# Optimization experiments

Hardware: AMD Instinct MI355X
Metric: run time of the kernel (lower is better)

## Reference

```python
import jax, jax.numpy as jnp
import numpy as np
from jax import lax

RADIUS = 0.25
MAX_NUM_NEIGHBORS = 32
N = 8192
D = 3
NUM_BATCHES = 16


def setup_inputs() -> dict:
    key = jax.random.key(0)
    k1, k2 = jax.random.split(key)
    x = jax.random.uniform(k1, (N, D), dtype=jnp.float32)  # points in unit cube
    batch = jnp.sort(jax.random.randint(k2, (N,), 0, NUM_BATCHES, dtype=jnp.int32))
    return {"x": x, "batch": batch}


def reference(x, batch):
    # radius_graph(x, r, max_num_neighbors=K, batch=batch):
    # for each target point i, up to K source points j (j != i, same batch,
    # ||x_i - x_j|| <= r). Deterministic tie-break: keep the K nearest.
    # Output padded to fixed shape [2, N*K] with -1 for missing edges.
    K = MAX_NUM_NEIGHBORS
    n = x.shape[0]
    sq = jnp.sum(x * x, axis=-1)                      # [N]
    d2 = sq[:, None] + sq[None, :] - 2.0 * (x @ x.T)  # [N, N] squared dists
    same_batch = batch[:, None] == batch[None, :]
    not_self = ~jnp.eye(n, dtype=bool)
    valid = same_batch & not_self & (d2 <= RADIUS * RADIUS)
    masked = jnp.where(valid, d2, jnp.inf)
    neg_vals, idx = lax.top_k(-masked, K)             # K nearest per row
    sel_valid = jnp.isfinite(neg_vals)                # [N, K]
    src = jnp.where(sel_valid, idx, -1)               # neighbor (source) index
    tgt = jnp.where(sel_valid,
                    jnp.broadcast_to(jnp.arange(n, dtype=idx.dtype)[:, None], (n, K)),
                    -1)
    # flow = source_to_target: row 0 = sources (neighbors), row 1 = targets
    edge_index = jnp.stack([src.reshape(-1), tgt.reshape(-1)], axis=0)  # [2, N*K]
    return edge_index
```

## Files before the change

### kernel.cpp

```cpp
#include <hip/hip_runtime.h>
#include <stdint.h>

#define NB   16
#define K    32
#define R2   0.0625f
#define WPB  4
#define MAXC 256

__global__ void radius_prep_kernel(const float* __restrict__ x,
                                   const int* __restrict__ batch,
                                   int n,
                                   int* __restrict__ starts,
                                   float* __restrict__ sq) {
#pragma clang fp contract(off)
    int i = blockIdx.x * blockDim.x + threadIdx.x;
    if (i >= n) return;
    float x0 = x[i * 3 + 0];
    float x1 = x[i * 3 + 1];
    float x2 = x[i * 3 + 2];
    float p0 = x0 * x0;
    float p1 = x1 * x1;
    float p2 = x2 * x2;
    sq[i] = (p0 + p1) + p2;

    int b  = batch[i];
    int bp = (i == 0) ? -1 : batch[i - 1];
    for (int bb = bp + 1; bb <= b; ++bb) starts[bb] = i;
    if (i == n - 1) {
        for (int bb = b + 1; bb <= NB; ++bb) starts[bb] = n;
    }
}

__global__ __launch_bounds__(256) void radius_knn_wave(
    const float* __restrict__ x,
    const int* __restrict__ batch,
    const int* __restrict__ starts,
    const float* __restrict__ sq,
    int n,
    int* __restrict__ out,
    int row_stride ) {
#pragma clang fp contract(off)
    __shared__ uint64_t buf[WPB][MAXC];
    __shared__ int      res[WPB][K];

    const int tid  = threadIdx.x;
    const int lane = tid & 63;
    const int wid  = tid >> 6;
    const int i    = blockIdx.x * WPB + wid;

    const int b = batch[i];
    const int s = starts[b];
    const int e = starts[b + 1];

    const float xi0 = x[i * 3 + 0];
    const float xi1 = x[i * 3 + 1];
    const float xi2 = x[i * 3 + 2];
    const float sqi = sq[i];

    const int range = e - s;
    const int iters = (range + 63) >> 6;
    int cbase = 0;
    for (int it = 0; it < iters; ++it) {
        const int j  = s + it * 64 + lane;
        const int jc = (j < e) ? j : s;
        float y0 = x[jc * 3 + 0];
        float y1 = x[jc * 3 + 1];
        float y2 = x[jc * 3 + 2];
        float dot = xi0 * y0;
        dot = fmaf(xi1, y1, dot);
        dot = fmaf(xi2, y2, dot);
        float d2 = (sqi + sq[jc]) - 2.0f * dot;
        bool pass = (j < e) && (j != i) && (d2 <= R2);

        d2 = d2 + 0.0f;
        uint32_t u = __float_as_uint(d2);
        u = (u & 0x80000000u) ? ~u : (u | 0x80000000u);
        uint64_t key = ((uint64_t)u << 32) | (uint32_t)jc;

        uint64_t mask = __ballot(pass);
        if (pass) {
            int off = cbase + __popcll(mask & ((1ull << lane) - 1ull));
            if (off < MAXC) buf[wid][off] = key;
        }
        cbase += (int)__popcll(mask);
    }
    int cnt = cbase < MAXC ? cbase : MAXC;
    const int nsel = cnt < K ? cnt : K;

    __syncthreads();

    for (int p = lane; p < cnt; p += 64) {
        uint64_t kp = buf[wid][p];
        int r = 0;
        for (int q = 0; q < cnt; ++q)
            r += (buf[wid][q] < kp) ? 1 : 0;
        if (r < K) res[wid][r] = (int)(uint32_t)(kp & 0xffffffffu);
    }

    __syncthreads();

    const long base = (long)i * K;
    if (lane < K) {
        out[base + lane] = (lane < nsel) ? res[wid][lane] : -1;
    } else {
        const int l2 = lane - K;
        out[row_stride + base + l2] = (l2 < nsel) ? i : -1;
    }
}

extern "C" void kernel_launch(void* const* d_in, const int* in_sizes, int n_in,
                              void* d_out, int out_size, void* d_ws, size_t ws_size,
                              hipStream_t stream) {
    const float* x     = (const float*)d_in[0];
    const int*   batch = (const int*)d_in[1];
    const int    n     = in_sizes[1];
    int*         out   = (int*)d_out;
    const int row_stride = out_size / 2;

    int*   starts = (int*)d_ws;
    float* sq     = (float*)((char*)d_ws + 128);

    radius_prep_kernel<<<(n + 255) / 256, 256, 0, stream>>>(x, batch, n, starts, sq);

    const int blocks = n / WPB;
    radius_knn_wave<<<blocks, 256, 0, stream>>>(x, batch, starts, sq, n,
                                                out, row_stride);
}
```

Measured before the change: 17.66 us.

## Fuse prep kernel into main kernel via binary search and inline squared norms

Removes the separate prep kernel launch that computed per-point squared norms and batch start offsets. Each wave now binary-searches the sorted batch array to find its batch range, and squared norms are recomputed on the fly from the coordinates. This saves a kernel launch and the dependency between the two kernels. In exchange it adds redundant per-wave search work and extra ALU work in the inner loop.

```diff
diff --git a/kernel.cpp b/kernel.cpp
--- a/kernel.cpp
+++ b/kernel.cpp
@@ -7,35 +7,9 @@
 #define WPB  4
 #define MAXC 256
 
-__global__ void radius_prep_kernel(const float* __restrict__ x,
-                                   const int* __restrict__ batch,
-                                   int n,
-                                   int* __restrict__ starts,
-                                   float* __restrict__ sq) {
-#pragma clang fp contract(off)
-    int i = blockIdx.x * blockDim.x + threadIdx.x;
-    if (i >= n) return;
-    float x0 = x[i * 3 + 0];
-    float x1 = x[i * 3 + 1];
-    float x2 = x[i * 3 + 2];
-    float p0 = x0 * x0;
-    float p1 = x1 * x1;
-    float p2 = x2 * x2;
-    sq[i] = (p0 + p1) + p2;
-
-    int b  = batch[i];
-    int bp = (i == 0) ? -1 : batch[i - 1];
-    for (int bb = bp + 1; bb <= b; ++bb) starts[bb] = i;
-    if (i == n - 1) {
-        for (int bb = b + 1; bb <= NB; ++bb) starts[bb] = n;
-    }
-}
-
-__global__ __launch_bounds__(256) void radius_knn_wave(
+__global__ __launch_bounds__(256) void radius_knn_fused(
     const float* __restrict__ x,
     const int* __restrict__ batch,
-    const int* __restrict__ starts,
-    const float* __restrict__ sq,
     int n,
     int* __restrict__ out,
     int row_stride ) {
@@ -49,13 +23,25 @@
     const int i    = blockIdx.x * WPB + wid;
 
     const int b = batch[i];
-    const int s = starts[b];
-    const int e = starts[b + 1];
+
+    int lo = 0, hi = n;
+    while (lo < hi) {
+        int mid = (lo + hi) >> 1;
+        if (batch[mid] < b) lo = mid + 1; else hi = mid;
+    }
+    const int s = lo;
+    int lo2 = s, hi2 = n;
+    while (lo2 < hi2) {
+        int mid = (lo2 + hi2) >> 1;
+        if (batch[mid] <= b) lo2 = mid + 1; else hi2 = mid;
+    }
+    const int e = lo2;
 
     const float xi0 = x[i * 3 + 0];
     const float xi1 = x[i * 3 + 1];
     const float xi2 = x[i * 3 + 2];
-    const float sqi = sq[i];
+    const float q0 = xi0 * xi0, q1 = xi1 * xi1, q2 = xi2 * xi2;
+    const float sqi = (q0 + q1) + q2;
 
     const int range = e - s;
     const int iters = (range + 63) >> 6;
@@ -66,10 +52,12 @@
         float y0 = x[jc * 3 + 0];
         float y1 = x[jc * 3 + 1];
         float y2 = x[jc * 3 + 2];
+        float p0 = y0 * y0, p1 = y1 * y1, p2 = y2 * y2;
+        float sqj = (p0 + p1) + p2;
         float dot = xi0 * y0;
         dot = fmaf(xi1, y1, dot);
         dot = fmaf(xi2, y2, dot);
-        float d2 = (sqi + sq[jc]) - 2.0f * dot;
+        float d2 = (sqi + sqj) - 2.0f * dot;
         bool pass = (j < e) && (j != i) && (d2 <= R2);
 
         d2 = d2 + 0.0f;
@@ -117,12 +105,6 @@
     int*         out   = (int*)d_out;
     const int row_stride = out_size / 2;
 
-    int*   starts = (int*)d_ws;
-    float* sq     = (float*)((char*)d_ws + 128);
-
-    radius_prep_kernel<<<(n + 255) / 256, 256, 0, stream>>>(x, batch, n, starts, sq);
-
     const int blocks = n / WPB;
-    radius_knn_wave<<<blocks, 256, 0, stream>>>(x, batch, starts, sq, n,
-                                                out, row_stride);
+    radius_knn_fused<<<blocks, 256, 0, stream>>>(x, batch, n, out, row_stride);
 }
```

Result: faster. 15.39 us (-12.9%).
